# Optimization experiments

Measured on AMD Instinct MI355X. Metric: run time of the kernel, lower is better.

## Reference

```python
import jax, jax.numpy as jnp
import numpy as np

NUM_HEADS = 16
MASKED_BIAS = -10000.0


def setup_inputs() -> dict:
    key = jax.random.key(0)
    k1, k2, k3 = jax.random.split(key, 3)
    B, S, D = 4, 2048, 1024
    return {
        "hidden_states": jax.random.normal(k1, (B, S, D), dtype=jnp.float32),
        "attention_mask": jnp.ones((B, S), dtype=jnp.float32),
        "w_attn": jax.random.normal(k2, (D, 3 * D), dtype=jnp.float32) * 0.02,
        "b_attn": jax.random.normal(k3, (3 * D,), dtype=jnp.float32) * 0.1,
    }


def reference(hidden_states, attention_mask, w_attn, b_attn):
    B, S, D = hidden_states.shape
    H = NUM_HEADS
    Dh = D // H
    # Conv1D: x @ W + b  -> [B, S, 3D]
    qkv = hidden_states @ w_attn + b_attn
    q, k, v = jnp.split(qkv, 3, axis=-1)

    def split_heads(t):  # [B,S,D] -> [B,H,S,Dh]
        return t.reshape(B, S, H, Dh).transpose(0, 2, 1, 3)

    q, k, v = split_heads(q), split_heads(k), split_heads(v)
    present = jnp.stack([k, v], axis=0)  # concat_key_value

    # process_mask: (1 - mask) * -10000, broadcast [B,1,1,S]
    add_mask = (1.0 - attention_mask)[:, None, None, :] * MASKED_BIAS

    qk = jnp.einsum("bhqd,bhkd->bhqk", q, k)
    norm_qk = qk * (1.0 / float(Dh) ** 0.5)
    causal = jnp.tril(jnp.ones((S, S), dtype=bool))[None, None]
    attn_weights = jnp.where(causal, norm_qk, jnp.asarray(MASKED_BIAS, norm_qk.dtype))
    attn_weights = attn_weights + add_mask
    probs = jax.nn.softmax(attn_weights, axis=-1)
    attn_output = jnp.einsum("bhqk,bhkd->bhqd", probs, v)
    # merge heads -> [B,S,D]
    attn_output = attn_output.transpose(0, 2, 1, 3).reshape(B, S, D)
    return attn_output, present
```

## Files before the change

kernel.cpp:

```cpp
#include <hip/hip_runtime.h>
#include <stdint.h>


#define B_SZ    4
#define S_LEN   2048
#define D_MODEL 1024
#define N3      3072
#define H_NUM   16
#define DH      64
#define M_TOT   8192

typedef __attribute__((ext_vector_type(8))) short short8;
typedef __attribute__((ext_vector_type(4))) float f32x4;

__device__ __forceinline__ unsigned short f2b(float f) {
  union { float f; unsigned int u; } x;
  x.f = f;
  unsigned int u = x.u;
  u += 0x7fffu + ((u >> 16) & 1u);
  return (unsigned short)(u >> 16);
}

__device__ __forceinline__ void async16(const void* g, void* l) {
  __builtin_amdgcn_global_load_lds((const __attribute__((address_space(1))) void*)g,
                                   (__attribute__((address_space(3))) void*)l,
                                   16, 0, 0);
}

__global__ void k_convert_x(const float* __restrict__ X, unsigned short* __restrict__ Xb) {
  const int i = (blockIdx.x * 256 + threadIdx.x) * 4;
  const float4 v = *(const float4*)(X + i);
  ushort4 o;
  o.x = f2b(v.x); o.y = f2b(v.y); o.z = f2b(v.z); o.w = f2b(v.w);
  *(ushort4*)(Xb + i) = o;
}

__global__ void k_wt(const float* __restrict__ W, unsigned short* __restrict__ Wt) {
  __shared__ float tile[32][33];
  const int n0 = blockIdx.x * 32, k0 = blockIdx.y * 32;
  const int tx = threadIdx.x, ty = threadIdx.y;
  for (int i = 0; i < 32; i += 8)
    tile[ty + i][tx] = W[(size_t)(k0 + ty + i) * N3 + n0 + tx];
  __syncthreads();
  for (int i = 0; i < 32; i += 8)
    Wt[(size_t)(n0 + ty + i) * D_MODEL + k0 + tx] = f2b(tile[tx][ty + i]);
}

__global__ __launch_bounds__(256) void k_gemm_qkv(
    const unsigned short* __restrict__ Xb, const unsigned short* __restrict__ Wt,
    const float* __restrict__ bias,
    unsigned short* __restrict__ Qb, unsigned short* __restrict__ Kb,
    float* __restrict__ presK, float* __restrict__ presV) {
  __shared__ __align__(16) unsigned short As[128 * 32];
  __shared__ __align__(16) unsigned short Bs[128 * 32];
  const int t = threadIdx.x;
  const int lane = t & 63, wave = t >> 6;
  const int g = lane >> 4, c = lane & 15;
  const int m0 = blockIdx.y * 128, n0 = blockIdx.x * 128;
  const int wm = (wave >> 1) * 64, wn = (wave & 1) * 64;

  const f32x4 zero = {0.f, 0.f, 0.f, 0.f};
  f32x4 acc[4][4];
  for (int i = 0; i < 4; ++i)
    for (int j = 0; j < 4; ++j) acc[i][j] = zero;

  const int row_a = t >> 2;
  const int col_a = (t & 3) * 8;
  const unsigned short* gA = Xb + (size_t)(m0 + row_a) * D_MODEL + col_a;
  const unsigned short* gB = Wt + (size_t)(n0 + row_a) * D_MODEL + col_a;
  const int wbase = wave * 1024;

  for (int k0 = 0; k0 < D_MODEL; k0 += 32) {
    __syncthreads();
    async16(gA + k0,                (char*)As + wbase);
    async16(gA + k0 + 64 * D_MODEL, (char*)As + 4096 + wbase);
    async16(gB + k0,                (char*)Bs + wbase);
    async16(gB + k0 + 64 * D_MODEL, (char*)Bs + 4096 + wbase);
    __syncthreads();

    short8 af[4], bf[4];
    for (int mi = 0; mi < 4; ++mi)
      af[mi] = *(const short8*)(As + (wm + mi * 16 + c) * 32 + g * 8);
    for (int ni = 0; ni < 4; ++ni)
      bf[ni] = *(const short8*)(Bs + (wn + ni * 16 + c) * 32 + g * 8);
    for (int mi = 0; mi < 4; ++mi)
      for (int ni = 0; ni < 4; ++ni)
        acc[mi][ni] = __builtin_amdgcn_mfma_f32_16x16x32_bf16(af[mi], bf[ni], acc[mi][ni], 0, 0, 0);
  }

  for (int ni = 0; ni < 4; ++ni) {
    const int n = n0 + wn + ni * 16 + c;
    const float bv = bias[n];
    const int sec = n >> 10;
    const int d = n & 1023;
    const int h = d >> 6, dh = d & 63;
    for (int mi = 0; mi < 4; ++mi) {
      for (int r = 0; r < 4; ++r) {
        const int m = m0 + wm + mi * 16 + g * 4 + r;
        const int b = m >> 11, s = m & 2047;
        const float val = acc[mi][ni][r] + bv;
        const size_t hidx = ((size_t)((b * H_NUM + h) * S_LEN + s)) * DH + dh;
        if (sec == 0) {
          Qb[hidx] = f2b(val);
        } else if (sec == 1) {
          presK[hidx] = val;
          Kb[hidx] = f2b(val);
        } else {
          presV[hidx] = val;
        }
      }
    }
  }
}

__global__ __launch_bounds__(256) void k_vt(const float* __restrict__ presV,
                                            unsigned short* __restrict__ Vt) {
  __shared__ unsigned short tile[64 * 72];
  const int t = threadIdx.x;
  const int bh = blockIdx.y;
  const int s0 = blockIdx.x * 64;
  const int row = t >> 2;
  const int dh0 = (t & 3) * 16;
  const float* src = presV + ((size_t)bh * S_LEN + s0 + row) * DH + dh0;
  for (int i = 0; i < 4; ++i) {
    const float4 v = *(const float4*)(src + i * 4);
    const int dh = dh0 + i * 4;
    tile[(dh + 0) * 72 + row] = f2b(v.x);
    tile[(dh + 1) * 72 + row] = f2b(v.y);
    tile[(dh + 2) * 72 + row] = f2b(v.z);
    tile[(dh + 3) * 72 + row] = f2b(v.w);
  }
  __syncthreads();
  const int dh = t >> 2, sc0 = (t & 3) * 16;
  unsigned short* dst = Vt + ((size_t)bh * DH + dh) * S_LEN + s0 + sc0;
  short8 o0, o1;
  for (int i = 0; i < 8; ++i) {
    o0[i] = (short)tile[dh * 72 + sc0 + i];
    o1[i] = (short)tile[dh * 72 + sc0 + 8 + i];
  }
  *(short8*)(dst) = o0;
  *(short8*)(dst + 8) = o1;
}

__global__ __launch_bounds__(512) void k_flash(
    const unsigned short* __restrict__ Qb, const unsigned short* __restrict__ Kb,
    const unsigned short* __restrict__ Vt, const float* __restrict__ mask,
    float* __restrict__ out) {
  __shared__ __align__(16) unsigned short Ks[64 * 64];
  __shared__ __align__(16) unsigned short Vs[64 * 64];
  __shared__ __align__(16) unsigned short Ps[8][16 * 72];
  const int t = threadIdx.x;
  const int lane = t & 63, wave = t >> 6;
  const int g = lane >> 4, c = lane & 15;
  const int bh = blockIdx.y;
  const int b = bh >> 4, h = bh & 15;
  const int srow = t >> 3;
  const int schunk = (t & 7) ^ (srow & 7);
  const unsigned short* gK0 = Kb + ((size_t)bh * S_LEN + srow) * DH + schunk * 8;
  const unsigned short* gV0 = Vt + ((size_t)bh * DH + srow) * S_LEN + schunk * 8;
  char* ldsK = (char*)Ks + wave * 1024;
  char* ldsV = (char*)Vs + wave * 1024;
  unsigned short* ps = &Ps[wave][0];
  const int sw_w = g * 8;
  const int sw_r = (c >> 2) * 8;
  const int kslot = (c & 7);

  for (int phase = 0; phase < 2; ++phase) {
    const int x = phase ? 15 - (int)blockIdx.x : (int)blockIdx.x;
    const int qb = x * 128;
    const int qw = qb + wave * 16;

    short8 aq[2];
    const size_t qoff = ((size_t)bh * S_LEN + qw) * DH;
    for (int kc = 0; kc < 2; ++kc)
      aq[kc] = *(const short8*)(Qb + qoff + (size_t)c * DH + kc * 32 + g * 8);

    const f32x4 zero = {0.f, 0.f, 0.f, 0.f};
    float m_i[4], l_i[4];
    f32x4 o_acc[4];
    for (int r = 0; r < 4; ++r) { m_i[r] = -1e30f; l_i[r] = 0.f; }
    for (int u = 0; u < 4; ++u) o_acc[u] = zero;

    for (int kb = 0; kb < qb + 128; kb += 64) {
      __syncthreads();
      async16(gK0 + (size_t)kb * DH, ldsK);
      async16(gV0 + kb, ldsV);
      __syncthreads();

      f32x4 sc[4];
      for (int ks = 0; ks < 4; ++ks) sc[ks] = zero;
      for (int ks = 0; ks < 4; ++ks) {
        const int krow = ks * 16 + c;
        for (int kc = 0; kc < 2; ++kc) {
          const short8 bk = *(const short8*)(Ks + krow * 64 + (((kc * 4 + g) ^ kslot) * 8));
          sc[ks] = __builtin_amdgcn_mfma_f32_16x16x32_bf16(aq[kc], bk, sc[ks], 0, 0, 0);
        }
      }

      float am[4];
      for (int ks = 0; ks < 4; ++ks)
        am[ks] = (1.0f - mask[b * S_LEN + kb + ks * 16 + c]) * -10000.0f;
      for (int r = 0; r < 4; ++r) {
        const int qrow = qw + g * 4 + r;
        for (int ks = 0; ks < 4; ++ks) {
          const int kcol = kb + ks * 16 + c;
          float v = sc[ks][r] * 0.125f;
          if (kcol > qrow) v = -10000.0f;
          sc[ks][r] = v + am[ks];
        }
      }

      for (int r = 0; r < 4; ++r) {
        float mx = fmaxf(fmaxf(sc[0][r], sc[1][r]), fmaxf(sc[2][r], sc[3][r]));
        for (int off = 1; off < 16; off <<= 1) mx = fmaxf(mx, __shfl_xor(mx, off));
        const float mnew = fmaxf(m_i[r], mx);
        const float alpha = __expf(m_i[r] - mnew);
        m_i[r] = mnew;
        float rs = 0.f;
        for (int ks = 0; ks < 4; ++ks) {
          const float p = __expf(sc[ks][r] - mnew);
          sc[ks][r] = p;
          rs += p;
        }
        for (int off = 1; off < 16; off <<= 1) rs += __shfl_xor(rs, off);
        l_i[r] = l_i[r] * alpha + rs;
        for (int u = 0; u < 4; ++u) o_acc[u][r] *= alpha;
      }

      for (int r = 0; r < 4; ++r) {
        const int ql = g * 4 + r;
        for (int ks = 0; ks < 4; ++ks)
          ps[ql * 72 + ((ks * 16 + c) ^ sw_w)] = f2b(sc[ks][r]);
      }
      short8 ap[2];
      for (int kc = 0; kc < 2; ++kc)
        ap[kc] = *(const short8*)(ps + c * 72 + ((kc * 32 + g * 8) ^ sw_r));

      for (int u = 0; u < 4; ++u) {
        const int vrow = u * 16 + c;
        for (int kc = 0; kc < 2; ++kc) {
          const short8 bv = *(const short8*)(Vs + vrow * 64 + (((kc * 4 + g) ^ kslot) * 8));
          o_acc[u] = __builtin_amdgcn_mfma_f32_16x16x32_bf16(ap[kc], bv, o_acc[u], 0, 0, 0);
        }
      }
    }

    for (int r = 0; r < 4; ++r) {
      const float inv = 1.0f / l_i[r];
      const int srow_o = qw + g * 4 + r;
      float* orow = out + ((size_t)(b * S_LEN + srow_o)) * D_MODEL + h * DH;
      for (int u = 0; u < 4; ++u)
        orow[u * 16 + c] = o_acc[u][r] * inv;
    }
  }
}

extern "C" void kernel_launch(void* const* d_in, const int* in_sizes, int n_in,
                              void* d_out, int out_size, void* d_ws, size_t ws_size,
                              hipStream_t stream) {
  const float* X    = (const float*)d_in[0];
  const float* mask = (const float*)d_in[1];
  const float* W    = (const float*)d_in[2];
  const float* bias = (const float*)d_in[3];

  float* out   = (float*)d_out;
  float* presK = out + (size_t)M_TOT * D_MODEL;
  float* presV = presK + (size_t)M_TOT * D_MODEL;

  char* ws = (char*)d_ws;
  unsigned short* Xb = (unsigned short*)(ws);
  unsigned short* Wt = (unsigned short*)(ws + 16777216);
  unsigned short* Qb = (unsigned short*)(ws + 23068672);
  unsigned short* Kb = (unsigned short*)(ws + 39845888);
  unsigned short* Vt = (unsigned short*)(ws + 56623104);

  k_convert_x<<<dim3(8192), dim3(256), 0, stream>>>(X, Xb);
  k_wt<<<dim3(96, 32), dim3(32, 8), 0, stream>>>(W, Wt);
  k_gemm_qkv<<<dim3(24, 64), dim3(256), 0, stream>>>(Xb, Wt, bias, Qb, Kb, presK, presV);
  k_vt<<<dim3(32, 64), dim3(256), 0, stream>>>(presV, Vt);
  k_flash<<<dim3(8, 64), dim3(512), 0, stream>>>(Qb, Kb, Vt, mask, out);
}
```

Before: 338.1 us.

## Restructure flash attention: transposed S, register P, double-buffered K/V, exp2 softmax

Reworks the flash-attention kernel to compute S transposed (K as the A operand, Q as B), so each lane owns one query row. That lets P be packed straight into bf16 registers for the PV MFMA (16x16x16) with no LDS round trip. K/V tiles are double-buffered with async global-to-LDS loads and explicit waitcnt and barriers, fully masked tiles above the diagonal are skipped per wave, and the causal check runs only on diagonal tiles. Softmax switches to exp2 with pre-scaled constants, the mask is precomputed into LDS once per block, and output stores become float4. This removes the P LDS staging, the per-element shuffle reductions and the serialized load-then-compute stall, at the cost of more LDS and hand-written sync that is fragile.

```diff
diff --git a/kernel.cpp b/kernel.cpp
--- a/kernel.cpp
+++ b/kernel.cpp
@@ -11,7 +11,12 @@
 #define M_TOT   8192
 
 typedef __attribute__((ext_vector_type(8))) short short8;
+typedef __attribute__((ext_vector_type(4))) short bf16x4;
 typedef __attribute__((ext_vector_type(4))) float f32x4;
+
+#define LOG2E      1.4426950408889634f
+#define SCL2E      0.18033688011112042f
+#define MASKB2     (-14426.9504f)
 
 __device__ __forceinline__ unsigned short f2b(float f) {
   union { float f; unsigned int u; } x;
@@ -19,6 +24,29 @@
   unsigned int u = x.u;
   u += 0x7fffu + ((u >> 16) & 1u);
   return (unsigned short)(u >> 16);
+}
+
+__device__ __forceinline__ unsigned int cvt_pk_bf16(float lo, float hi) {
+  unsigned int r;
+  asm("v_cvt_pk_bf16_f32 %0, %1, %2" : "=v"(r) : "v"(lo), "v"(hi));
+  return r;
+}
+
+__device__ __forceinline__ float exp2_fast(float x) {
+#if __has_builtin(__builtin_amdgcn_exp2f)
+  return __builtin_amdgcn_exp2f(x);
+#else
+  return __expf(x * 0.6931471805599453f);
+#endif
+}
+
+__device__ __forceinline__ f32x4 mfma16(bf16x4 a, bf16x4 b, f32x4 c) {
+#if __has_builtin(__builtin_amdgcn_mfma_f32_16x16x16bf16_1k)
+  return __builtin_amdgcn_mfma_f32_16x16x16bf16_1k(a, b, c, 0, 0, 0);
+#else
+  asm("v_mfma_f32_16x16x16_bf16 %0, %1, %2, %0" : "+v"(c) : "v"(a), "v"(b));
+  return c;
+#endif
 }
 
 __device__ __forceinline__ void async16(const void* g, void* l) {
@@ -146,9 +174,9 @@
     const unsigned short* __restrict__ Qb, const unsigned short* __restrict__ Kb,
     const unsigned short* __restrict__ Vt, const float* __restrict__ mask,
     float* __restrict__ out) {
-  __shared__ __align__(16) unsigned short Ks[64 * 64];
-  __shared__ __align__(16) unsigned short Vs[64 * 64];
-  __shared__ __align__(16) unsigned short Ps[8][16 * 72];
+  __shared__ __align__(16) unsigned short Ks[2][64 * 64];
+  __shared__ __align__(16) unsigned short Vs[2][64 * 64];
+  __shared__ __align__(16) float Ams[S_LEN];
   const int t = threadIdx.x;
   const int lane = t & 63, wave = t >> 6;
   const int g = lane >> 4, c = lane & 15;
@@ -158,99 +186,141 @@
   const int schunk = (t & 7) ^ (srow & 7);
   const unsigned short* gK0 = Kb + ((size_t)bh * S_LEN + srow) * DH + schunk * 8;
   const unsigned short* gV0 = Vt + ((size_t)bh * DH + srow) * S_LEN + schunk * 8;
-  char* ldsK = (char*)Ks + wave * 1024;
-  char* ldsV = (char*)Vs + wave * 1024;
-  unsigned short* ps = &Ps[wave][0];
-  const int sw_w = g * 8;
-  const int sw_r = (c >> 2) * 8;
-  const int kslot = (c & 7);
+  const int kslot = c & 7;
+
+  {
+    const float4 mv = *(const float4*)(mask + (size_t)b * S_LEN + t * 4);
+    float4 o;
+    o.x = (1.0f - mv.x) * MASKB2;
+    o.y = (1.0f - mv.y) * MASKB2;
+    o.z = (1.0f - mv.z) * MASKB2;
+    o.w = (1.0f - mv.w) * MASKB2;
+    *(float4*)(Ams + t * 4) = o;
+  }
+
+  const f32x4 zero = {0.f, 0.f, 0.f, 0.f};
 
   for (int phase = 0; phase < 2; ++phase) {
     const int x = phase ? 15 - (int)blockIdx.x : (int)blockIdx.x;
     const int qb = x * 128;
     const int qw = qb + wave * 16;
-
-    short8 aq[2];
+    const int qrow = qw + c;
+
+    short8 bq[2];
     const size_t qoff = ((size_t)bh * S_LEN + qw) * DH;
+#pragma unroll
     for (int kc = 0; kc < 2; ++kc)
-      aq[kc] = *(const short8*)(Qb + qoff + (size_t)c * DH + kc * 32 + g * 8);
-
-    const f32x4 zero = {0.f, 0.f, 0.f, 0.f};
-    float m_i[4], l_i[4];
+      bq[kc] = *(const short8*)(Qb + qoff + (size_t)c * DH + kc * 32 + g * 8);
+
+    float m_i = -1e30f, l_i = 0.f;
     f32x4 o_acc[4];
-    for (int r = 0; r < 4; ++r) { m_i[r] = -1e30f; l_i[r] = 0.f; }
-    for (int u = 0; u < 4; ++u) o_acc[u] = zero;
-
-    for (int kb = 0; kb < qb + 128; kb += 64) {
-      __syncthreads();
-      async16(gK0 + (size_t)kb * DH, ldsK);
-      async16(gV0 + kb, ldsV);
-      __syncthreads();
-
-      f32x4 sc[4];
-      for (int ks = 0; ks < 4; ++ks) sc[ks] = zero;
-      for (int ks = 0; ks < 4; ++ks) {
-        const int krow = ks * 16 + c;
-        for (int kc = 0; kc < 2; ++kc) {
-          const short8 bk = *(const short8*)(Ks + krow * 64 + (((kc * 4 + g) ^ kslot) * 8));
-          sc[ks] = __builtin_amdgcn_mfma_f32_16x16x32_bf16(aq[kc], bk, sc[ks], 0, 0, 0);
-        }
+#pragma unroll
+    for (int dt = 0; dt < 4; ++dt) o_acc[dt] = zero;
+
+    const int nt = (qb + 128) >> 6;
+    async16(gK0, (char*)(&Ks[0][0]) + wave * 1024);
+    async16(gV0, (char*)(&Vs[0][0]) + wave * 1024);
+
+    for (int tt = 0; tt < nt; ++tt) {
+      const int kb = tt << 6;
+      const int cur = tt & 1;
+      if (tt + 1 < nt) {
+        async16(gK0 + (size_t)(kb + 64) * DH, (char*)(&Ks[cur ^ 1][0]) + wave * 1024);
+        async16(gV0 + (kb + 64),              (char*)(&Vs[cur ^ 1][0]) + wave * 1024);
+        asm volatile("s_waitcnt vmcnt(2) lgkmcnt(0)" ::: "memory");
+      } else {
+        asm volatile("s_waitcnt vmcnt(0) lgkmcnt(0)" ::: "memory");
       }
-
-      float am[4];
-      for (int ks = 0; ks < 4; ++ks)
-        am[ks] = (1.0f - mask[b * S_LEN + kb + ks * 16 + c]) * -10000.0f;
-      for (int r = 0; r < 4; ++r) {
-        const int qrow = qw + g * 4 + r;
+      __builtin_amdgcn_s_barrier();
+      __builtin_amdgcn_sched_barrier(0);
+
+      if (qw + 16 > kb) {
+        const unsigned short* ks_base = &Ks[cur][0];
+        const unsigned short* vs_base = &Vs[cur][0];
+
+        f32x4 sc[4];
+#pragma unroll
         for (int ks = 0; ks < 4; ++ks) {
-          const int kcol = kb + ks * 16 + c;
-          float v = sc[ks][r] * 0.125f;
-          if (kcol > qrow) v = -10000.0f;
-          sc[ks][r] = v + am[ks];
+          f32x4 a = zero;
+          const int krow = ks * 16 + c;
+#pragma unroll
+          for (int kc = 0; kc < 2; ++kc) {
+            const short8 ak = *(const short8*)(ks_base + krow * 64 + (((kc * 4 + g) ^ kslot) * 8));
+            a = __builtin_amdgcn_mfma_f32_16x16x32_bf16(ak, bq[kc], a, 0, 0, 0);
+          }
+          sc[ks] = a;
+        }
+
+        const bool need_causal = (kb + 63 > qw);
+        float mxk[4];
+#pragma unroll
+        for (int ks = 0; ks < 4; ++ks) {
+          const float4 amv = *(const float4*)(Ams + kb + ks * 16 + g * 4);
+          float am4[4];
+          am4[0] = amv.x; am4[1] = amv.y; am4[2] = amv.z; am4[3] = amv.w;
+#pragma unroll
+          for (int r = 0; r < 4; ++r) {
+            float v = sc[ks][r] * SCL2E + am4[r];
+            if (need_causal && (kb + ks * 16 + g * 4 + r > qrow))
+              v = MASKB2 + am4[r];
+            sc[ks][r] = v;
+          }
+          mxk[ks] = fmaxf(fmaxf(sc[ks][0], sc[ks][1]), fmaxf(sc[ks][2], sc[ks][3]));
+        }
+
+        float mx = fmaxf(fmaxf(mxk[0], mxk[1]), fmaxf(mxk[2], mxk[3]));
+        mx = fmaxf(mx, __shfl_xor(mx, 16));
+        mx = fmaxf(mx, __shfl_xor(mx, 32));
+        const float mnew = fmaxf(m_i, mx);
+        const float alpha = exp2_fast(m_i - mnew);
+        m_i = mnew;
+
+        bf16x4 pk[4];
+        float rsk[4];
+#pragma unroll
+        for (int ks = 0; ks < 4; ++ks) {
+          const float p0 = exp2_fast(sc[ks][0] - mnew);
+          const float p1 = exp2_fast(sc[ks][1] - mnew);
+          const float p2 = exp2_fast(sc[ks][2] - mnew);
+          const float p3 = exp2_fast(sc[ks][3] - mnew);
+          rsk[ks] = (p0 + p1) + (p2 + p3);
+          union { unsigned int u[2]; bf16x4 v4; } pu;
+          pu.u[0] = cvt_pk_bf16(p0, p1);
+          pu.u[1] = cvt_pk_bf16(p2, p3);
+          pk[ks] = pu.v4;
+        }
+        float rs = (rsk[0] + rsk[1]) + (rsk[2] + rsk[3]);
+        rs += __shfl_xor(rs, 16);
+        rs += __shfl_xor(rs, 32);
+        l_i = l_i * alpha + rs;
+#pragma unroll
+        for (int dt = 0; dt < 4; ++dt) o_acc[dt] *= alpha;
+
+#pragma unroll
+        for (int dt = 0; dt < 4; ++dt) {
+          const int vrow = dt * 16 + c;
+#pragma unroll
+          for (int ks = 0; ks < 4; ++ks) {
+            const bf16x4 av = *(const bf16x4*)(vs_base + vrow * 64 +
+                (((2 * ks + (g >> 1)) ^ kslot) * 8) + (g & 1) * 4);
+            o_acc[dt] = mfma16(av, pk[ks], o_acc[dt]);
+          }
         }
       }
-
-      for (int r = 0; r < 4; ++r) {
-        float mx = fmaxf(fmaxf(sc[0][r], sc[1][r]), fmaxf(sc[2][r], sc[3][r]));
-        for (int off = 1; off < 16; off <<= 1) mx = fmaxf(mx, __shfl_xor(mx, off));
-        const float mnew = fmaxf(m_i[r], mx);
-        const float alpha = __expf(m_i[r] - mnew);
-        m_i[r] = mnew;
-        float rs = 0.f;
-        for (int ks = 0; ks < 4; ++ks) {
-          const float p = __expf(sc[ks][r] - mnew);
-          sc[ks][r] = p;
-          rs += p;
-        }
-        for (int off = 1; off < 16; off <<= 1) rs += __shfl_xor(rs, off);
-        l_i[r] = l_i[r] * alpha + rs;
-        for (int u = 0; u < 4; ++u) o_acc[u][r] *= alpha;
-      }
-
-      for (int r = 0; r < 4; ++r) {
-        const int ql = g * 4 + r;
-        for (int ks = 0; ks < 4; ++ks)
-          ps[ql * 72 + ((ks * 16 + c) ^ sw_w)] = f2b(sc[ks][r]);
-      }
-      short8 ap[2];
-      for (int kc = 0; kc < 2; ++kc)
-        ap[kc] = *(const short8*)(ps + c * 72 + ((kc * 32 + g * 8) ^ sw_r));
-
-      for (int u = 0; u < 4; ++u) {
-        const int vrow = u * 16 + c;
-        for (int kc = 0; kc < 2; ++kc) {
-          const short8 bv = *(const short8*)(Vs + vrow * 64 + (((kc * 4 + g) ^ kslot) * 8));
-          o_acc[u] = __builtin_amdgcn_mfma_f32_16x16x32_bf16(ap[kc], bv, o_acc[u], 0, 0, 0);
-        }
-      }
+      __builtin_amdgcn_sched_barrier(0);
+      __builtin_amdgcn_s_barrier();
     }
 
-    for (int r = 0; r < 4; ++r) {
-      const float inv = 1.0f / l_i[r];
-      const int srow_o = qw + g * 4 + r;
-      float* orow = out + ((size_t)(b * S_LEN + srow_o)) * D_MODEL + h * DH;
-      for (int u = 0; u < 4; ++u)
-        orow[u * 16 + c] = o_acc[u][r] * inv;
+    const float inv = 1.0f / l_i;
+    float* orow = out + ((size_t)(b * S_LEN + qrow)) * D_MODEL + h * DH;
+#pragma unroll
+    for (int dt = 0; dt < 4; ++dt) {
+      float4 o;
+      o.x = o_acc[dt][0] * inv;
+      o.y = o_acc[dt][1] * inv;
+      o.z = o_acc[dt][2] * inv;
+      o.w = o_acc[dt][3] * inv;
+      *(float4*)(orow + dt * 16 + g * 4) = o;
     }
   }
 }
```

Measured after the change: 306.8 us. -9.3%, faster.
